# Kernel optimization log

Measured on AMD Instinct MI355X. Metric: run time of the kernel, lower is better.

## Reference

```python
import jax, jax.numpy as jnp
import numpy as np

N, D, H = 2048, 1024, 16
HD = D // H  # 64
SCALE = float(np.sqrt(HD))  # sqrt(features // heads) = 8.0


def setup_inputs() -> dict:
    key = jax.random.key(0)
    ks = jax.random.split(key, 9)
    s = 0.02
    return {
        "x": jax.random.normal(ks[0], (N, D), dtype=jnp.float32),
        "Wq": jax.random.normal(ks[1], (D, D), dtype=jnp.float32) * s,
        "bq": jnp.zeros((D,), dtype=jnp.float32),
        "Wk": jax.random.normal(ks[2], (D, D), dtype=jnp.float32) * s,
        "bk": jnp.zeros((D,), dtype=jnp.float32),
        "Wv": jax.random.normal(ks[3], (D, D), dtype=jnp.float32) * s,
        "bv": jnp.zeros((D,), dtype=jnp.float32),
        "Wo": jax.random.normal(ks[4], (D, D), dtype=jnp.float32) * s,
        "bo": jnpp if False else jnp.zeros((D,), dtype=jnp.float32),
    }


def reference(x, Wq, bq, Wk, bk, Wv, bv, Wo, bo):
    # projections: [n, d]
    q = x @ Wq + bq
    k = x @ Wk + bk
    v = x @ Wv + bv
    # split heads: n (h d) -> h n d
    def split(t):
        return t.reshape(N, H, HD).transpose(1, 0, 2)
    q, k, v = split(q), split(k), split(v)
    # attention scores [h, n, n]
    scores = jnp.einsum('hnd,hmd->hnm', q, k) / SCALE
    # causal mask (tril), fill with dtype min as in original
    dmin = jnp.finfo(scores.dtype).min
    mask = jnp.tril(jnp.ones((N, N), dtype=bool))
    scores = jnp.where(mask, scores, dmin)
    attn = jax.nn.softmax(scores, axis=-1)
    # weighted sum, merge heads: h n d -> n (h d)
    out = jnp.einsum('hnm,hmd->hnd', attn, v)
    out = out.transpose(1, 0, 2).reshape(N, D)
    return out @ Wo + bo
```

## Files before the change

### kernel.cpp

```cpp
#include <hip/hip_runtime.h>
#include <hip/hip_bf16.h>
#include <math.h>

#define SA_N 2048
#define SA_D 1024
#define SA_H 16
#define SA_HD 64

typedef __attribute__((ext_vector_type(8))) short bf16x8;
typedef __attribute__((ext_vector_type(4))) float f32x4;
typedef __attribute__((address_space(3))) void lds_t;
typedef __attribute__((address_space(1))) void gmem_t;

#define SC2 0.18033688011112042f

__global__ __launch_bounds__(256) void prep_kernel(
    const float* __restrict__ x,
    const float* __restrict__ Wq, const float* __restrict__ Wk,
    const float* __restrict__ Wv, const float* __restrict__ Wo,
    __hip_bfloat16* __restrict__ xbf, __hip_bfloat16* __restrict__ WtAll)
{
    const int tid = threadIdx.x;
    const int z = blockIdx.z;
    if (z < 2) {
        const int r = z * 1024 + blockIdx.y * 32 + (tid >> 3);
        const int c = blockIdx.x * 32 + (tid & 7) * 4;
        const size_t idx = (size_t)r * SA_D + c;
        float4 v = *reinterpret_cast<const float4*>(&x[idx]);
        union { __hip_bfloat16 hh[4]; short4 s4; } u;
        u.hh[0] = __float2bfloat16(v.x);
        u.hh[1] = __float2bfloat16(v.y);
        u.hh[2] = __float2bfloat16(v.z);
        u.hh[3] = __float2bfloat16(v.w);
        *reinterpret_cast<short4*>(&xbf[idx]) = u.s4;
    } else {
        const int w = z - 2;
        const float* W = (w == 0) ? Wq : (w == 1) ? Wk : (w == 2) ? Wv : Wo;
        const float scale = (w == 0) ? SC2 : 1.0f;
        __hip_bfloat16* Wt = WtAll + (size_t)w * SA_D * SA_D;
        __shared__ float t[32][33];
        const int c0 = blockIdx.x * 32, r0 = blockIdx.y * 32;
        const int tx = tid & 31, ty = tid >> 5;
#pragma unroll
        for (int p = 0; p < 4; ++p)
            t[ty + p * 8][tx] = W[(size_t)(r0 + ty + p * 8) * SA_D + c0 + tx] * scale;
        __syncthreads();
#pragma unroll
        for (int p = 0; p < 4; ++p)
            Wt[(size_t)(c0 + ty + p * 8) * SA_D + r0 + tx] =
                __float2bfloat16(t[tx][ty + p * 8]);
    }
}

__global__ __launch_bounds__(256) void gemm_qkv_kernel(
    const __hip_bfloat16* __restrict__ xbf, const __hip_bfloat16* __restrict__ WtAll,
    const float* __restrict__ bq, const float* __restrict__ bk, const float* __restrict__ bv,
    __hip_bfloat16* __restrict__ Qb, __hip_bfloat16* __restrict__ Kb,
    __hip_bfloat16* __restrict__ VtT)
{
    __shared__ __align__(16) char As[64 * 128];
    __shared__ __align__(16) char Bs[3][32 * 128];

    const int tid = threadIdx.x;
    const int wave = tid >> 6, lane = tid & 63;
    const int m = lane & 15, quad = lane >> 4;
    const int wm = wave >> 1, wn = wave & 1;
    const int row0 = blockIdx.y * 64, col0 = blockIdx.x * 32;

    f32x4 acc[3][2];
#pragma unroll
    for (int w = 0; w < 3; ++w)
#pragma unroll
        for (int mi = 0; mi < 2; ++mi) acc[w][mi] = (f32x4){0.f, 0.f, 0.f, 0.f};

    const int sr = tid >> 3;
    const int sc = tid & 7;

    for (int k0 = 0; k0 < SA_D; k0 += 64) {
#pragma unroll
        for (int p = 0; p < 2; ++p) {
            const int r = p * 32 + sr;
            const int pc = (sc ^ (r & 7)) * 16;
            const char* ga = (const char*)(xbf + (size_t)(row0 + r) * SA_D + k0) + pc;
            __builtin_amdgcn_global_load_lds((gmem_t*)ga,
                (lds_t*)(As + p * 4096 + wave * 1024), 16, 0, 0);
        }
#pragma unroll
        for (int w = 0; w < 3; ++w) {
            const int pc = (sc ^ (sr & 7)) * 16;
            const char* gb = (const char*)(WtAll + (size_t)w * SA_D * SA_D
                                           + (size_t)(col0 + sr) * SA_D + k0) + pc;
            __builtin_amdgcn_global_load_lds((gmem_t*)gb,
                (lds_t*)(Bs[w] + wave * 1024), 16, 0, 0);
        }
        __syncthreads();

#pragma unroll
        for (int s = 0; s < 2; ++s) {
            bf16x8 af[2];
#pragma unroll
            for (int mi = 0; mi < 2; ++mi) {
                const int row = wm * 32 + mi * 16 + m;
                const int pc = (s * 4 + quad) ^ (row & 7);
                af[mi] = *reinterpret_cast<const bf16x8*>(As + row * 128 + pc * 16);
            }
            const int rb = wn * 16 + m;
            const int pcb = (s * 4 + quad) ^ (rb & 7);
#pragma unroll
            for (int w = 0; w < 3; ++w) {
                bf16x8 bf = *reinterpret_cast<const bf16x8*>(Bs[w] + rb * 128 + pcb * 16);
#pragma unroll
                for (int mi = 0; mi < 2; ++mi)
                    acc[w][mi] = __builtin_amdgcn_mfma_f32_16x16x32_bf16(
                        af[mi], bf, acc[w][mi], 0, 0, 0);
            }
        }
        __syncthreads();
    }

    const int col = col0 + wn * 16 + m;
    const float bvq = bq[col] * SC2, bvk = bk[col], bvv = bv[col];
#pragma unroll
    for (int mi = 0; mi < 2; ++mi) {
        const int rbase = row0 + wm * 32 + mi * 16 + quad * 4;
#pragma unroll
        for (int reg = 0; reg < 4; ++reg) {
            Qb[(size_t)(rbase + reg) * SA_D + col] = __float2bfloat16(acc[0][mi][reg] + bvq);
            Kb[(size_t)(rbase + reg) * SA_D + col] = __float2bfloat16(acc[1][mi][reg] + bvk);
        }
        union { __hip_bfloat16 hh[4]; short4 s4; } u;
#pragma unroll
        for (int reg = 0; reg < 4; ++reg)
            u.hh[reg] = __float2bfloat16(acc[2][mi][reg] + bvv);
        *reinterpret_cast<short4*>(&VtT[(size_t)col * SA_N + rbase]) = u.s4;
    }
}

__global__ __launch_bounds__(256) void gemm_out_kernel(
    const __hip_bfloat16* __restrict__ A, const __hip_bfloat16* __restrict__ Bt,
    const float* __restrict__ bias, float* __restrict__ Cout)
{
    __shared__ __align__(16) char As[64 * 128];
    __shared__ __align__(16) char Bs[64 * 128];
    const int tid = threadIdx.x;
    const int wave = tid >> 6, lane = tid & 63;
    const int m = lane & 15, quad = lane >> 4;
    const int wm = wave >> 1, wn = wave & 1;
    const int row0 = blockIdx.y * 64, col0 = blockIdx.x * 64;

    f32x4 acc[2][2];
#pragma unroll
    for (int i = 0; i < 2; ++i)
#pragma unroll
        for (int j = 0; j < 2; ++j) acc[i][j] = (f32x4){0.f, 0.f, 0.f, 0.f};

    const int sr = tid >> 3;
    const int sc = tid & 7;

    for (int k0 = 0; k0 < SA_D; k0 += 64) {
#pragma unroll
        for (int p = 0; p < 2; ++p) {
            const int r = p * 32 + sr;
            const int pc = (sc ^ (r & 7)) * 16;
            const char* ga = (const char*)(A + (size_t)(row0 + r) * SA_D + k0) + pc;
            __builtin_amdgcn_global_load_lds((gmem_t*)ga,
                (lds_t*)(As + p * 4096 + wave * 1024), 16, 0, 0);
            const char* gb = (const char*)(Bt + (size_t)(col0 + r) * SA_D + k0) + pc;
            __builtin_amdgcn_global_load_lds((gmem_t*)gb,
                (lds_t*)(Bs + p * 4096 + wave * 1024), 16, 0, 0);
        }
        __syncthreads();

#pragma unroll
        for (int s = 0; s < 2; ++s) {
            bf16x8 af[2], bfr[2];
#pragma unroll
            for (int mi = 0; mi < 2; ++mi) {
                const int row = wm * 32 + mi * 16 + m;
                const int pc = (s * 4 + quad) ^ (row & 7);
                af[mi] = *reinterpret_cast<const bf16x8*>(As + row * 128 + pc * 16);
            }
#pragma unroll
            for (int ni = 0; ni < 2; ++ni) {
                const int col = wn * 32 + ni * 16 + m;
                const int pc = (s * 4 + quad) ^ (col & 7);
                bfr[ni] = *reinterpret_cast<const bf16x8*>(Bs + col * 128 + pc * 16);
            }
#pragma unroll
            for (int mi = 0; mi < 2; ++mi)
#pragma unroll
                for (int ni = 0; ni < 2; ++ni)
                    acc[mi][ni] = __builtin_amdgcn_mfma_f32_16x16x32_bf16(
                        af[mi], bfr[ni], acc[mi][ni], 0, 0, 0);
        }
        __syncthreads();
    }

#pragma unroll
    for (int ni = 0; ni < 2; ++ni) {
        const int col = col0 + wn * 32 + ni * 16 + m;
        const float bv = bias[col];
#pragma unroll
        for (int mi = 0; mi < 2; ++mi) {
            const int rbase = row0 + wm * 32 + mi * 16 + quad * 4;
#pragma unroll
            for (int reg = 0; reg < 4; ++reg)
                Cout[(size_t)(rbase + reg) * SA_D + col] = acc[mi][ni][reg] + bv;
        }
    }
}

__global__ __launch_bounds__(512, 4) void flash_mfma_kernel(
    const __hip_bfloat16* __restrict__ Qb,
    const __hip_bfloat16* __restrict__ Kb,
    const __hip_bfloat16* __restrict__ Vt,
    __hip_bfloat16* __restrict__ O)
{
    const int b = blockIdx.x;
    const int h = b & 15;
    const int qraw = b >> 4;
    const int qt = (qraw < 16) ? qraw : 47 - qraw;
    const int row0 = qt * 64;
    const int ntiles = (qt >> 1) + 1;

    const int tid = threadIdx.x;
    const int wave = tid >> 6, lane = tid & 63;
    const int g = wave >> 2, w4 = wave & 3;
    const int ln = lane & 15, quad = lane >> 4;

    __shared__ __align__(16) char Qs[64 * 128];
    __shared__ __align__(16) char Ks[128 * 128];
    __shared__ __align__(16) char Vs[64 * 256];
    __shared__ __align__(16) char Ps[2][64 * 144];
    __shared__ float lmerge[64];

    {
        const int r = wave * 8 + (lane >> 3);
        const int pc = ((lane & 7) ^ (r & 7)) * 16;
        const char* gq = (const char*)(Qb + (size_t)(row0 + r) * SA_D + h * SA_HD) + pc;
        __builtin_amdgcn_global_load_lds((gmem_t*)gq,
            (lds_t*)(Qs + wave * 1024), 16, 0, 0);
    }

    f32x4 oacc[4], lacc;
#pragma unroll
    for (int dg = 0; dg < 4; ++dg) oacc[dg] = (f32x4){0.f, 0.f, 0.f, 0.f};
    lacc = (f32x4){0.f, 0.f, 0.f, 0.f};

    const short one_bf = (short)0x3F80;
    const bf16x8 ones = {one_bf, one_bf, one_bf, one_bf, one_bf, one_bf, one_bf, one_bf};

    for (int kt = 0; kt < ntiles; ++kt) {
        __syncthreads();
#pragma unroll
        for (int p = 0; p < 2; ++p) {
            const int r = p * 64 + wave * 8 + (lane >> 3);
            const int pc = ((lane & 7) ^ (r & 7)) * 16;
            const char* gk = (const char*)(Kb + (size_t)(kt * 128 + r) * SA_D + h * SA_HD) + pc;
            __builtin_amdgcn_global_load_lds((gmem_t*)gk,
                (lds_t*)(Ks + p * 8192 + wave * 1024), 16, 0, 0);
        }
#pragma unroll
        for (int p = 0; p < 2; ++p) {
            const int r = p * 32 + wave * 4 + (lane >> 4);
            const int pc = ((lane & 15) ^ (r & 15)) * 16;
            const char* gv = (const char*)(Vt + (size_t)(h * SA_HD + r) * SA_N + kt * 128) + pc;
            __builtin_amdgcn_global_load_lds((gmem_t*)gv,
                (lds_t*)(Vs + p * 8192 + wave * 1024), 16, 0, 0);
        }
        __syncthreads();

        f32x4 sacc[4];
#pragma unroll
        for (int gg = 0; gg < 4; ++gg) sacc[gg] = (f32x4){0.f, 0.f, 0.f, 0.f};
        const int mrow = w4 * 16 + ln;
#pragma unroll
        for (int s = 0; s < 2; ++s) {
            const int pca = (s * 4 + quad) ^ (mrow & 7);
            bf16x8 af = *reinterpret_cast<const bf16x8*>(Qs + mrow * 128 + pca * 16);
#pragma unroll
            for (int gg = 0; gg < 4; ++gg) {
                const int krow = g * 64 + gg * 16 + ln;
                const int pcb = (s * 4 + quad) ^ (krow & 7);
                bf16x8 bf = *reinterpret_cast<const bf16x8*>(Ks + krow * 128 + pcb * 16);
                sacc[gg] = __builtin_amdgcn_mfma_f32_16x16x32_bf16(af, bf, sacc[gg], 0, 0, 0);
            }
        }

        const bool last = (kt == ntiles - 1);
        const int prow_b = w4 * 16 + quad * 4;
        const int qrow_b = row0 + prow_b;
        char* Pg = Ps[g];
#pragma unroll
        for (int gg = 0; gg < 4; ++gg) {
            const int key = kt * 128 + g * 64 + gg * 16 + ln;
#pragma unroll
            for (int reg = 0; reg < 4; ++reg) {
                float p = exp2f(sacc[gg][reg]);
                if (last && key > (qrow_b + reg)) p = 0.f;
                *reinterpret_cast<__hip_bfloat16*>(
                    Pg + (prow_b + reg) * 144 + (gg * 16 + ln) * 2) = __float2bfloat16(p);
            }
        }

#pragma unroll
        for (int s2 = 0; s2 < 2; ++s2) {
            bf16x8 pf = *reinterpret_cast<const bf16x8*>(
                Pg + (w4 * 16 + ln) * 144 + s2 * 64 + quad * 16);
            lacc = __builtin_amdgcn_mfma_f32_16x16x32_bf16(pf, ones, lacc, 0, 0, 0);
#pragma unroll
            for (int dg = 0; dg < 4; ++dg) {
                const int vrow = dg * 16 + ln;
                const int kc = g * 8 + s2 * 4 + quad;
                const int pcb = (kc ^ (vrow & 15)) * 16;
                bf16x8 vf = *reinterpret_cast<const bf16x8*>(Vs + vrow * 256 + pcb);
                oacc[dg] = __builtin_amdgcn_mfma_f32_16x16x32_bf16(pf, vf, oacc[dg], 0, 0, 0);
            }
        }
    }

    __syncthreads();
    float* Kf = reinterpret_cast<float*>(Ks);
    if (g == 1) {
#pragma unroll
        for (int reg = 0; reg < 4; ++reg) {
            const int row = w4 * 16 + quad * 4 + reg;
#pragma unroll
            for (int dg = 0; dg < 4; ++dg)
                Kf[row * 64 + dg * 16 + ln] = oacc[dg][reg];
            if (ln == 0) lmerge[row] = lacc[reg];
        }
    }
    __syncthreads();
    if (g == 0) {
#pragma unroll
        for (int reg = 0; reg < 4; ++reg) {
            const int row = w4 * 16 + quad * 4 + reg;
            const float inv = 1.0f / (lacc[reg] + lmerge[row]);
            const int qrow = row0 + row;
#pragma unroll
            for (int dg = 0; dg < 4; ++dg)
                O[(size_t)qrow * SA_D + h * SA_HD + dg * 16 + ln] =
                    __float2bfloat16((oacc[dg][reg] + Kf[row * 64 + dg * 16 + ln]) * inv);
        }
    }
}

extern "C" void kernel_launch(void* const* d_in, const int* in_sizes, int n_in,
                              void* d_out, int out_size, void* d_ws, size_t ws_size,
                              hipStream_t stream) {
    const float* x  = (const float*)d_in[0];
    const float* Wq = (const float*)d_in[1];
    const float* bq = (const float*)d_in[2];
    const float* Wk = (const float*)d_in[3];
    const float* bk = (const float*)d_in[4];
    const float* Wv = (const float*)d_in[5];
    const float* bv = (const float*)d_in[6];
    const float* Wo = (const float*)d_in[7];
    const float* bo = (const float*)d_in[8];
    float* out = (float*)d_out;

    const size_t ND = (size_t)SA_N * SA_D;
    const size_t DD = (size_t)SA_D * SA_D;
    __hip_bfloat16* xbf   = (__hip_bfloat16*)d_ws;
    __hip_bfloat16* WtAll = xbf + ND;
    __hip_bfloat16* Qb    = WtAll + 4 * DD;
    __hip_bfloat16* Kb    = Qb + ND;
    __hip_bfloat16* VtT   = Kb + ND;
    __hip_bfloat16* Abf   = VtT + ND;

    prep_kernel<<<dim3(32, 32, 6), 256, 0, stream>>>(x, Wq, Wk, Wv, Wo, xbf, WtAll);
    gemm_qkv_kernel<<<dim3(SA_D / 32, SA_N / 64), 256, 0, stream>>>(
        xbf, WtAll, bq, bk, bv, Qb, Kb, VtT);
    flash_mfma_kernel<<<dim3(512), 512, 0, stream>>>(Qb, Kb, VtT, Abf);
    gemm_out_kernel<<<dim3(SA_D / 64, SA_N / 64), 256, 0, stream>>>(
        Abf, WtAll + 3 * DD, bo, out);
}
```

Before: 144.1 us.

## Keep P in registers by computing transposed scores, permuting V layout

The flash kernel now computes S^T (K as A operand, Q fragments held in registers), so each lane's exp'd scores directly form the A-operand fragment for the PV MFMA. This removes the Q and P LDS buffers and the LDS round-trip for P. The V transpose store in the QKV projection is permuted to match the new key ordering inside the fragment. Row sums move from an MFMA against ones to a scalar accumulation plus cross-lane shuffles. Launch bounds are raised to allow more resident blocks given the smaller LDS footprint, which may add register pressure.

```diff
diff --git a/kernel.cpp b/kernel.cpp
--- a/kernel.cpp
+++ b/kernel.cpp
@@ -132,7 +132,8 @@
 #pragma unroll
         for (int reg = 0; reg < 4; ++reg)
             u.hh[reg] = __float2bfloat16(acc[2][mi][reg] + bvv);
-        *reinterpret_cast<short4*>(&VtT[(size_t)col * SA_N + rbase]) = u.s4;
+        *reinterpret_cast<short4*>(
+            &VtT[(size_t)col * SA_N + row0 + mi * 32 + quad * 8 + wm * 4]) = u.s4;
     }
 }
 
@@ -210,7 +211,7 @@
     }
 }
 
-__global__ __launch_bounds__(512, 4) void flash_mfma_kernel(
+__global__ __launch_bounds__(512, 6) void flash_mfma_kernel(
     const __hip_bfloat16* __restrict__ Qb,
     const __hip_bfloat16* __restrict__ Kb,
     const __hip_bfloat16* __restrict__ Vt,
@@ -228,27 +229,20 @@
     const int g = wave >> 2, w4 = wave & 3;
     const int ln = lane & 15, quad = lane >> 4;
 
-    __shared__ __align__(16) char Qs[64 * 128];
     __shared__ __align__(16) char Ks[128 * 128];
     __shared__ __align__(16) char Vs[64 * 256];
-    __shared__ __align__(16) char Ps[2][64 * 144];
-    __shared__ float lmerge[64];
-
-    {
-        const int r = wave * 8 + (lane >> 3);
-        const int pc = ((lane & 7) ^ (r & 7)) * 16;
-        const char* gq = (const char*)(Qb + (size_t)(row0 + r) * SA_D + h * SA_HD) + pc;
-        __builtin_amdgcn_global_load_lds((gmem_t*)gq,
-            (lds_t*)(Qs + wave * 1024), 16, 0, 0);
-    }
-
-    f32x4 oacc[4], lacc;
+    __shared__ float lm[2][64];
+
+    bf16x8 qf[2];
+#pragma unroll
+    for (int s = 0; s < 2; ++s)
+        qf[s] = *reinterpret_cast<const bf16x8*>(
+            Qb + (size_t)(row0 + w4 * 16 + ln) * SA_D + h * SA_HD + s * 32 + quad * 8);
+
+    f32x4 oacc[4];
 #pragma unroll
     for (int dg = 0; dg < 4; ++dg) oacc[dg] = (f32x4){0.f, 0.f, 0.f, 0.f};
-    lacc = (f32x4){0.f, 0.f, 0.f, 0.f};
-
-    const short one_bf = (short)0x3F80;
-    const bf16x8 ones = {one_bf, one_bf, one_bf, one_bf, one_bf, one_bf, one_bf, one_bf};
+    float lsum = 0.f;
 
     for (int kt = 0; kt < ntiles; ++kt) {
         __syncthreads();
@@ -273,51 +267,56 @@
         f32x4 sacc[4];
 #pragma unroll
         for (int gg = 0; gg < 4; ++gg) sacc[gg] = (f32x4){0.f, 0.f, 0.f, 0.f};
-        const int mrow = w4 * 16 + ln;
 #pragma unroll
         for (int s = 0; s < 2; ++s) {
-            const int pca = (s * 4 + quad) ^ (mrow & 7);
-            bf16x8 af = *reinterpret_cast<const bf16x8*>(Qs + mrow * 128 + pca * 16);
 #pragma unroll
             for (int gg = 0; gg < 4; ++gg) {
                 const int krow = g * 64 + gg * 16 + ln;
                 const int pcb = (s * 4 + quad) ^ (krow & 7);
-                bf16x8 bf = *reinterpret_cast<const bf16x8*>(Ks + krow * 128 + pcb * 16);
-                sacc[gg] = __builtin_amdgcn_mfma_f32_16x16x32_bf16(af, bf, sacc[gg], 0, 0, 0);
+                bf16x8 af = *reinterpret_cast<const bf16x8*>(Ks + krow * 128 + pcb * 16);
+                sacc[gg] = __builtin_amdgcn_mfma_f32_16x16x32_bf16(af, qf[s], sacc[gg], 0, 0, 0);
             }
         }
 
         const bool last = (kt == ntiles - 1);
-        const int prow_b = w4 * 16 + quad * 4;
-        const int qrow_b = row0 + prow_b;
-        char* Pg = Ps[g];
+        const int qrow_g = row0 + w4 * 16 + ln;
+        __hip_bfloat16 ph[4][4];
 #pragma unroll
         for (int gg = 0; gg < 4; ++gg) {
-            const int key = kt * 128 + g * 64 + gg * 16 + ln;
+            const int keyb = kt * 128 + g * 64 + gg * 16 + quad * 4;
 #pragma unroll
             for (int reg = 0; reg < 4; ++reg) {
                 float p = exp2f(sacc[gg][reg]);
-                if (last && key > (qrow_b + reg)) p = 0.f;
-                *reinterpret_cast<__hip_bfloat16*>(
-                    Pg + (prow_b + reg) * 144 + (gg * 16 + ln) * 2) = __float2bfloat16(p);
-            }
-        }
+                if (last && (keyb + reg) > qrow_g) p = 0.f;
+                lsum += p;
+                ph[gg][reg] = __float2bfloat16(p);
+            }
+        }
+        bf16x8 pf[2];
+        union { __hip_bfloat16 hh[8]; bf16x8 v; } pu0, pu1;
+#pragma unroll
+        for (int reg = 0; reg < 4; ++reg) {
+            pu0.hh[reg] = ph[0][reg]; pu0.hh[4 + reg] = ph[2][reg];
+            pu1.hh[reg] = ph[1][reg]; pu1.hh[4 + reg] = ph[3][reg];
+        }
+        pf[0] = pu0.v; pf[1] = pu1.v;
 
 #pragma unroll
         for (int s2 = 0; s2 < 2; ++s2) {
-            bf16x8 pf = *reinterpret_cast<const bf16x8*>(
-                Pg + (w4 * 16 + ln) * 144 + s2 * 64 + quad * 16);
-            lacc = __builtin_amdgcn_mfma_f32_16x16x32_bf16(pf, ones, lacc, 0, 0, 0);
 #pragma unroll
             for (int dg = 0; dg < 4; ++dg) {
                 const int vrow = dg * 16 + ln;
                 const int kc = g * 8 + s2 * 4 + quad;
                 const int pcb = (kc ^ (vrow & 15)) * 16;
                 bf16x8 vf = *reinterpret_cast<const bf16x8*>(Vs + vrow * 256 + pcb);
-                oacc[dg] = __builtin_amdgcn_mfma_f32_16x16x32_bf16(pf, vf, oacc[dg], 0, 0, 0);
-            }
-        }
-    }
+                oacc[dg] = __builtin_amdgcn_mfma_f32_16x16x32_bf16(pf[s2], vf, oacc[dg], 0, 0, 0);
+            }
+        }
+    }
+
+    lsum += __shfl_xor(lsum, 16);
+    lsum += __shfl_xor(lsum, 32);
+    if (quad == 0) lm[g][w4 * 16 + ln] = lsum;
 
     __syncthreads();
     float* Kf = reinterpret_cast<float*>(Ks);
@@ -328,7 +327,6 @@
 #pragma unroll
             for (int dg = 0; dg < 4; ++dg)
                 Kf[row * 64 + dg * 16 + ln] = oacc[dg][reg];
-            if (ln == 0) lmerge[row] = lacc[reg];
         }
     }
     __syncthreads();
@@ -336,7 +334,7 @@
 #pragma unroll
         for (int reg = 0; reg < 4; ++reg) {
             const int row = w4 * 16 + quad * 4 + reg;
-            const float inv = 1.0f / (lacc[reg] + lmerge[row]);
+            const float inv = 1.0f / (lm[0][row] + lm[1][row]);
             const int qrow = row0 + row;
 #pragma unroll
             for (int dg = 0; dg < 4; ++dg)
```

After: 144.0 us. About the same (-0.1%).
